# Kernel tuning notes

Measured on AMD Instinct MI355X. Metric: run time of the kernel, lower is better.

The kernel has to match this reference:

```python
import jax, jax.numpy as jnp
import numpy as np

STEP, LEAK = 16, 32
KS = STEP + LEAK          # kernel_size = 48
FODEP = KS                # forced depression window
SYNAPSES, NEURONS = 64, 256
IC, OC = 1, 10
DENSE = 0.5
THETA = DENSE * SYNAPSES * IC   # 32.0
BIAS = 0.5
BATCH, TIME = 16, 512


def setup_inputs() -> dict:
    key = jax.random.key(0)
    k1, k2 = jax.random.split(key)
    # binary input spikes, density 0.2
    input_spikes = (jax.random.uniform(k1, (BATCH, IC, SYNAPSES, TIME)) < 0.2).astype(jnp.float32)
    # weight ~ Exponential(rate=1/w_init=2).sample().clip(0,1), mean 0.5
    u = jax.random.uniform(k2, (OC * NEURONS, IC * SYNAPSES), minval=1e-6, maxval=1.0)
    weight = jnp.clip(-0.5 * jnp.log(u), 0.0, 1.0)
    return {"input_spikes": input_spikes, "weight": weight}


def _step_fire_leak_kernel(weight):
    # kernel[o, i, t] = max(0, min(t/step, -(t - w*step)/leak + w)), flipped on t
    t = jnp.arange(KS, dtype=weight.dtype)
    t_spike = t / STEP                                        # rising edge
    t_leak = -(t - weight[..., None] * STEP) / LEAK + weight[..., None]  # decaying edge
    kernel = jnp.maximum(jnp.zeros((), weight.dtype), jnp.minimum(t_spike, t_leak))
    return kernel[..., ::-1]


def _forward(input_spikes, weight):
    B, C, S, T = input_spikes.shape
    x = input_spikes.reshape(B, C * S, T)
    kernel = _step_fire_leak_kernel(weight)                   # [OC*N, IC*S, KS]
    # conv1d with padding = kernel_size on both sides -> T' = T + KS + 1
    pot = jax.lax.conv_general_dilated(
        x, kernel, window_strides=(1,), padding=[(KS, KS)],
        dimension_numbers=("NCH", "OIH", "NCH"))
    Tp = pot.shape[-1]
    pot = pot.reshape(B, OC, NEURONS, Tp) + BIAS * THETA      # unsupervised bias path

    # winner-takes-all scan over time with per-(batch, neuron) depression counter
    pot_t = pot.transpose(3, 0, 2, 1)                         # [T', B, N, OC]
    dep0 = jnp.zeros((B, NEURONS, OC), jnp.int32)

    def step_fn(dep, p):
        masked = jnp.where(dep == 0, p, jnp.zeros((), p.dtype))
        winner = jnp.argmax(masked, axis=-1)                  # [B, N]
        wpot = jnp.take_along_axis(masked, winner[..., None], axis=-1)[..., 0]
        spike = (wpot > THETA).astype(p.dtype)                # [B, N]
        w_t = jax.nn.one_hot(winner, OC, dtype=p.dtype) * spike[..., None]
        dep = jnp.clip(dep + spike.astype(jnp.int32)[..., None] * FODEP - 1, 0, FODEP - 1)
        return dep, w_t

    _, winners = jax.lax.scan(step_fn, dep0, pot_t)           # [T', B, N, OC]
    return winners.transpose(1, 3, 2, 0)                      # [B, OC, N, T'] float


def reference(input_spikes, weight):
    return _forward(input_spikes, weight)
```

## Files before the change

### kernel.cpp

```cpp
#include <hip/hip_runtime.h>

#define B_   16
#define OC_  10
#define N_   256
#define O_   2560
#define S_   64
#define T_   512
#define KS_  48
#define TP_  561
#define TT   24
#define WROW 72

#define XROWS 624
#define SCH    16
#define CPITCH 572
#define KP     18

using i32x4 = __attribute__((ext_vector_type(4))) int;

__global__ void prep_all(const float* __restrict__ x, const float* __restrict__ w,
                         unsigned char* __restrict__ xb, signed char* __restrict__ Bg) {
    if (blockIdx.x < 512) {
#pragma unroll
        for (int it = 0; it < 4; ++it) {
            int idx = blockIdx.x * 256 + threadIdx.x + it * 131072;
            int t = idx & 511;
            int bi = idx >> 9;
            int i = bi & 63, b = bi >> 6;
            xb[((size_t)(b * 512 + t) << 6) + i] = (x[idx] != 0.0f) ? 1 : 0;
        }
    } else {
        int base = (blockIdx.x - 512) * 256 + threadIdx.x;
#pragma unroll
        for (int it = 0; it < 16; ++it) {
            int idx = base + it * 491520;
            int i = idx & 63;
            int oj = idx >> 6;
            int j = oj % KS_, o = oj / KS_;
            float wv = w[(o << 6) + i];
            float rise = (float)j * 0.0625f;
            float leak = -((float)j - wv * 16.0f) * 0.03125f + wv;
            float kv   = fmaxf(0.0f, fminf(rise, leak));
            int q  = (int)lrintf(kv * 4194304.0f);
            int d0 = ((q + 128) & 255) - 128;
            int q1 = (q - d0) >> 8;
            int d1 = ((q1 + 128) & 255) - 128;
            int d2 = (q1 - d1) >> 8;
            int oc = o >> 4, ol = o & 15;
            int jm = j & 15, jh = j >> 4;
            int pos = jm * 3 + jh;
            size_t bse = (((size_t)(oc * KS_ + pos) * 48) + ol) * 64 + i;
            Bg[bse]            = (signed char)d0;
            Bg[bse + 16 * 64]  = (signed char)d1;
            Bg[bse + 32 * 64]  = (signed char)d2;
        }
    }
}

__global__ __launch_bounds__(512, 2) void gemm_scan(
    const unsigned char* __restrict__ xb,
    const signed char*  __restrict__ Bg,
    float* __restrict__ out)
{
    __shared__ __align__(16) unsigned char smem[143616];
    unsigned char* xT    = smem;
    unsigned char* codeW = smem;
    float*         keyBB = (float*)(smem + 39936);
    unsigned char* codeBB = smem + 39936 + 82944;

    const int tid  = threadIdx.x;
    const int lane = tid & 63;
    const int wave = tid >> 6;
    const int tq   = wave >> 1;
    const int chh  = wave & 1;
    const int nc = blockIdx.x;
    const int b  = blockIdx.y;
    const int lrow = lane & 15;
    const int quad = lane >> 4;
    const int tw = tq * 144;

    float*         keyB  = keyBB + chh * (576 * KP);
    unsigned char* codeB = codeBB + chh * (576 * KP);

    const size_t SL = (size_t)KS_ * 48 * 64;
    const signed char* Bcur = Bg + (size_t)(chh * 80 + nc) * SL
                            + lrow * 64 + quad * 16;

    for (int z = tid; z < 112 * 4; z += 512) {
        int zi = z >> 2, p = z & 3;
        int r = (zi < 49) ? zi : (561 + zi - 49);
        *(i32x4*)(xT + r * 64 + p * 16) = (i32x4){0, 0, 0, 0};
    }
    const unsigned char* xbb = xb + ((size_t)b << 15);
    for (int q = tid; q < 2048; q += 512) {
        i32x4 v = *(const i32x4*)(xbb + q * 16);
        int t = q >> 2, p = q & 3;
        int r = 49 + t;
        *(i32x4*)(xT + r * 64 + ((p ^ ((r >> 1) & 3)) << 4)) = v;
    }

    i32x4 acc[9][3];
    i32x4 af[11], bfA[9], bfB[9];

#pragma unroll
    for (int jh = 0; jh < 3; ++jh)
#pragma unroll
        for (int f = 0; f < 3; ++f)
            bfA[jh * 3 + f] = *(const i32x4*)(Bcur + jh * 3072 + f * 1024);

    __syncthreads();

    {
        const int rb0 = tw + 16 + lrow;
        const int ca0 = ((quad ^ ((rb0 >> 1) & 3)) << 4);
#pragma unroll
        for (int k = 0; k < 11; ++k)
            af[k] = *(const i32x4*)(xT + (rb0 + k * 16) * 64 + ca0);
    }

#define MF(bfC, mi, jh, f)                                                    \
    acc[mi][f] = __builtin_amdgcn_mfma_i32_16x16x64_i8(                       \
        af[(mi) + 2 - (jh)], bfC[(jh) * 3 + (f)], acc[mi][f], 0, 0, 0)

#define PAIR(bfC, m0)                                                         \
    MF(bfC, m0, 0, 0); MF(bfC, m0, 0, 1); MF(bfC, m0, 0, 2);                  \
    MF(bfC, (m0)+1, 0, 0); MF(bfC, (m0)+1, 0, 1); MF(bfC, (m0)+1, 0, 2);      \
    MF(bfC, m0, 1, 0); MF(bfC, m0, 1, 1); MF(bfC, m0, 1, 2);                  \
    MF(bfC, (m0)+1, 1, 0); MF(bfC, (m0)+1, 1, 1); MF(bfC, (m0)+1, 1, 2);      \
    MF(bfC, m0, 2, 0); MF(bfC, m0, 2, 1); MF(bfC, m0, 2, 2);                  \
    MF(bfC, (m0)+1, 2, 0); MF(bfC, (m0)+1, 2, 1); MF(bfC, (m0)+1, 2, 2);

#define PAIR9(bfC)                                                            \
    MF(bfC, 8, 0, 0); MF(bfC, 8, 0, 1); MF(bfC, 8, 0, 2);                     \
    MF(bfC, 8, 1, 0); MF(bfC, 8, 1, 1); MF(bfC, 8, 1, 2);                     \
    MF(bfC, 8, 2, 0); MF(bfC, 8, 2, 1); MF(bfC, 8, 2, 2);

#define LDA_(row) (*(const i32x4*)(xT + (row) * 64 + coffN))
#define LDB_(BP, jh, f) (*(const i32x4*)((BP) + (tn3 + (jh)) * 3072 + (f) * 1024))

#define TLOC(T, bfC, bfN, BP) {                                               \
        const int rbn   = tw + 16 - (((T) + 1) & 15) + lrow;                  \
        const int coffN = ((quad ^ ((rbn >> 1) & 3)) << 4);                   \
        const int tn3   = (((T) + 1) & 15) * 3;                               \
        __builtin_amdgcn_s_setprio(1);                                        \
        PAIR(bfC, 0)                                                          \
        af[0] = LDA_(rbn);        af[1] = LDA_(rbn + 16);                     \
        bfN[0] = LDB_(BP, 0, 0); bfN[1] = LDB_(BP, 0, 1); bfN[2] = LDB_(BP, 0, 2); \
        PAIR(bfC, 2)                                                          \
        af[2] = LDA_(rbn + 32);   af[3] = LDA_(rbn + 48);                     \
        bfN[3] = LDB_(BP, 1, 0); bfN[4] = LDB_(BP, 1, 1); bfN[5] = LDB_(BP, 1, 2); \
        PAIR(bfC, 4)                                                          \
        af[4] = LDA_(rbn + 64);   af[5] = LDA_(rbn + 80);                     \
        bfN[6] = LDB_(BP, 2, 0); bfN[7] = LDB_(BP, 2, 1); bfN[8] = LDB_(BP, 2, 2); \
        PAIR(bfC, 6)                                                          \
        af[6] = LDA_(rbn + 96);   af[7] = LDA_(rbn + 112);                    \
        PAIR9(bfC)                                                            \
        af[8] = LDA_(rbn + 128);  af[9] = LDA_(rbn + 144);                    \
        af[10] = LDA_(rbn + 160);                                             \
        __builtin_amdgcn_s_setprio(0);                                        \
    }

    for (int c = 0; c < 5; ++c) {
        const signed char* Bnxt = (c == 4) ? Bcur : (Bcur + 16 * SL);

#pragma unroll
        for (int mi = 0; mi < 9; ++mi)
#pragma unroll
            for (int f = 0; f < 3; ++f)
                acc[mi][f] = (i32x4){0, 0, 0, 0};

        for (int tp = 0; tp < 7; ++tp) {
            TLOC(2 * tp,     bfA, bfB, Bcur)
            TLOC(2 * tp + 1, bfB, bfA, Bcur)
        }
        TLOC(14, bfA, bfB, Bcur)
        TLOC(15, bfB, bfA, Bnxt)

        {
            const unsigned char cv = (unsigned char)(chh * 5 + c + 1);
#pragma unroll
            for (int mi = 0; mi < 9; ++mi) {
#pragma unroll
                for (int r = 0; r < 4; ++r) {
                    int t = tw + mi * 16 + quad * 4 + r;
                    int pq_i = acc[mi][0][r] + (acc[mi][1][r] << 8)
                             + (acc[mi][2][r] << 16);
                    float pq = (float)pq_i * 2.384185791015625e-7f;
                    int ix = t * KP + lrow;
                    if (c == 0) {
                        keyB[ix] = pq; codeB[ix] = cv;
                    } else if (pq > keyB[ix]) {
                        keyB[ix] = pq; codeB[ix] = cv;
                    }
                }
            }
        }
        Bcur = Bnxt;
    }

#undef MF
#undef PAIR
#undef PAIR9
#undef LDA_
#undef LDB_
#undef TLOC

    __syncthreads();

    for (int ix = tid; ix < 576 * 16; ix += 512) {
        int t = ix >> 4, nl = ix & 15;
        if (t >= TP_) continue;
        int ip = t * KP + nl;
        float f0 = keyBB[ip];
        float f1 = keyBB[576 * KP + ip];
        float best = f0;
        unsigned char cd = codeBB[ip];
        if (f1 > f0) { best = f1; cd = codeBB[576 * KP + ip]; }
        codeW[nl * CPITCH + t] = ((best + 16.0f) > 32.0f) ? cd : (unsigned char)0;
    }
    __syncthreads();

    {
        const int ln = tid & 63;
        float* ob = out + (((size_t)b * OC_) * N_ + nc * SCH) * TP_;
        for (int nsel = wave; nsel < SCH; nsel += 8) {
            const unsigned char* cp = &codeW[nsel * CPITCH];
            int t = 0;
            while (t < TP_) {
                int tt = t + ln;
                unsigned char v = (tt < TP_) ? cp[tt] : (unsigned char)0;
                unsigned long long mask = __ballot(v != 0);
                if (mask == 0ULL) { t += 64; continue; }
                int k = (int)__builtin_ctzll(mask);
                if (ln == k)
                    ob[((size_t)(v - 1) * N_ + nsel) * TP_ + (t + k)] = 1.0f;
                t += k + KS_;
            }
        }
    }
}

__global__ void transpose_w(const float* __restrict__ w, float* __restrict__ wT) {
    int idx = blockIdx.x * 256 + threadIdx.x;
    if (idx >= O_ * S_) return;
    int o = idx >> 6, i = idx & 63;
    wT[i * O_ + o] = w[idx];
}

__global__ __launch_bounds__(256) void conv_kernel(
    const float* __restrict__ x, const float* __restrict__ wT,
    float* __restrict__ pot)
{
    const int b  = blockIdx.y;
    const int t0 = blockIdx.z * TT;
    const int o  = blockIdx.x * 256 + threadIdx.x;

    __shared__ __align__(16) float xsh[S_][WROW];
    for (int idx = threadIdx.x; idx < S_ * WROW; idx += 256) {
        int i = idx / WROW, m = idx - i * WROW;
        int t = t0 - KS_ + m;
        float v = 0.0f;
        if (t >= 0 && t < T_) v = x[(b * S_ + i) * T_ + t];
        xsh[i][m] = v;
    }
    __syncthreads();

    float acch[TT], accl[TT];
#pragma unroll
    for (int tl = 0; tl < TT; ++tl) { acch[tl] = 0.0f; accl[tl] = 0.0f; }

    for (int i = 0; i < S_; ++i) {
        float xw[WROW];
#pragma unroll
        for (int w4 = 0; w4 < WROW / 4; ++w4) {
            const float4 v = *reinterpret_cast<const float4*>(&xsh[i][w4 * 4]);
            xw[w4 * 4 + 0] = v.x; xw[w4 * 4 + 1] = v.y;
            xw[w4 * 4 + 2] = v.z; xw[w4 * 4 + 3] = v.w;
        }
        const float wv = wT[i * O_ + o];
#pragma unroll
        for (int j = 1; j < KS_; ++j) {
            float rise = (float)j * 0.0625f;
            float leak = -((float)j - wv * 16.0f) * 0.03125f + wv;
            float kv   = fmaxf(0.0f, fminf(rise, leak));
            float khi  = rintf(kv * 4096.0f) * 2.44140625e-4f;
            float klo  = kv - khi;
#pragma unroll
            for (int tl = 0; tl < TT; ++tl) {
                float xv = xw[tl + (KS_ - 1) - j];
                acch[tl] = fmaf(xv, khi, acch[tl]);
                accl[tl] = fmaf(xv, klo, accl[tl]);
            }
        }
    }
#pragma unroll
    for (int tl = 0; tl < TT; ++tl) {
        int t = t0 + tl;
        if (t < TP_) pot[((size_t)b * TP_ + t) * O_ + o] = acch[tl] + accl[tl];
    }
}

__global__ void scan_prep(const float* __restrict__ pot, unsigned char* __restrict__ code) {
    int idx = blockIdx.x * 256 + threadIdx.x;
    if (idx >= B_ * TP_ * N_) return;
    int n  = idx & (N_ - 1);
    int bt = idx >> 8;
    const float* p = pot + (size_t)bt * O_ + n;
    float best = p[0]; int bo = 0;
#pragma unroll
    for (int oc = 1; oc < OC_; ++oc) {
        float v = p[oc * N_];
        if (v > best) { best = v; bo = oc; }
    }
    code[idx] = ((best + 16.0f) > 32.0f) ? (unsigned char)(bo + 1) : (unsigned char)0;
}

__global__ void scan_run(const unsigned char* __restrict__ code, float* __restrict__ out) {
    int idx = blockIdx.x * 256 + threadIdx.x;
    if (idx >= B_ * N_) return;
    int b = idx >> 8, n = idx & 255;
    const unsigned char* c = code + (size_t)b * TP_ * N_ + n;
    int t = 0;
    while (t < TP_) {
        unsigned char buf[KS_];
#pragma unroll
        for (int k = 0; k < KS_; ++k) {
            int tt = t + k;
            buf[k] = (tt < TP_) ? c[(size_t)tt * N_] : (unsigned char)0;
        }
        int adv = KS_;
#pragma unroll
        for (int k = 0; k < KS_; ++k) {
            if (buf[k]) {
                out[(((size_t)b * OC_ + (buf[k] - 1)) * N_ + n) * TP_ + (t + k)] = 1.0f;
                adv = k + KS_;
                break;
            }
        }
        t += adv;
    }
}

extern "C" void kernel_launch(void* const* d_in, const int* in_sizes, int n_in,
                              void* d_out, int out_size, void* d_ws, size_t ws_size,
                              hipStream_t stream) {
    const float* x = (const float*)d_in[0];
    const float* w = (const float*)d_in[1];
    float* out = (float*)d_out;

    char* ws = (char*)d_ws;
    const size_t szX = (size_t)B_ * T_ * S_;
    const size_t szB = (size_t)160 * KS_ * 48 * 64;
    const size_t need = szX + szB;

    if (ws_size >= need) {
        unsigned char* xb  = (unsigned char*)ws;
        signed char* Bg    = (signed char*)(ws + szX);

        hipMemsetAsync(d_out, 0, (size_t)out_size * sizeof(float), stream);
        prep_all<<<2432, 256, 0, stream>>>(x, w, xb, Bg);
        gemm_scan<<<dim3(16, 16), 512, 0, stream>>>(xb, Bg, out);
    } else {
        size_t pot_bytes  = (size_t)B_ * TP_ * O_ * sizeof(float);
        size_t code_bytes = (size_t)B_ * TP_ * N_;
        float* pot = (float*)ws;
        unsigned char* code = (unsigned char*)(ws + pot_bytes);
        float* wT = (float*)(ws + pot_bytes + code_bytes);

        hipMemsetAsync(d_out, 0, (size_t)out_size * sizeof(float), stream);
        transpose_w<<<(O_ * S_ + 255) / 256, 256, 0, stream>>>(w, wT);
        conv_kernel<<<dim3(O_ / 256, B_, (TP_ + TT - 1) / TT), 256, 0, stream>>>(x, wT, pot);
        scan_prep<<<(B_ * TP_ * N_ + 255) / 256, 256, 0, stream>>>(pot, code);
        scan_run<<<(B_ * N_ + 255) / 256, 256, 0, stream>>>(code, out);
    }
}
```

Before: 238.9 us.

## Overlap per-chunk epilogue with next chunk MFMAs and fold output zeroing into prep

The max/argmax epilogue over accumulators for chunk c is moved into the first time-tile of chunk c+1, interleaved with MFMA pairs so LDS compare/store work overlaps with matrix math. keyB is now pre-initialized to a large negative value so every chunk uses the same compare path, and the final chunk's epilogue runs after the loop. Separately, the hipMemsetAsync of the output is replaced by extra blocks in prep_all that zero the output with vector stores, removing one launch. The interleaving raises register pressure and depends on the scheduler actually overlapping the work.

```diff
diff --git a/kernel.cpp b/kernel.cpp
--- a/kernel.cpp
+++ b/kernel.cpp
@@ -16,10 +16,13 @@
 #define CPITCH 572
 #define KP     18
 
+#define OUTF4  5744640
+
 using i32x4 = __attribute__((ext_vector_type(4))) int;
 
 __global__ void prep_all(const float* __restrict__ x, const float* __restrict__ w,
-                         unsigned char* __restrict__ xb, signed char* __restrict__ Bg) {
+                         unsigned char* __restrict__ xb, signed char* __restrict__ Bg,
+                         float* __restrict__ outz) {
     if (blockIdx.x < 512) {
 #pragma unroll
         for (int it = 0; it < 4; ++it) {
@@ -29,7 +32,7 @@
             int i = bi & 63, b = bi >> 6;
             xb[((size_t)(b * 512 + t) << 6) + i] = (x[idx] != 0.0f) ? 1 : 0;
         }
-    } else {
+    } else if (blockIdx.x < 2432) {
         int base = (blockIdx.x - 512) * 256 + threadIdx.x;
 #pragma unroll
         for (int it = 0; it < 16; ++it) {
@@ -54,6 +57,14 @@
             Bg[bse + 16 * 64]  = (signed char)d1;
             Bg[bse + 32 * 64]  = (signed char)d2;
         }
+    } else {
+        i32x4* o4 = (i32x4*)outz;
+        int base = (blockIdx.x - 2432) * 256 + threadIdx.x;
+#pragma unroll
+        for (int it = 0; it < 8; ++it) {
+            int idx = base + it * 737280;
+            if (idx < OUTF4) o4[idx] = (i32x4){0, 0, 0, 0};
+        }
     }
 }
 
@@ -86,6 +97,12 @@
     const signed char* Bcur = Bg + (size_t)(chh * 80 + nc) * SL
                             + lrow * 64 + quad * 16;
 
+#pragma unroll
+    for (int mi = 0; mi < 9; ++mi)
+#pragma unroll
+        for (int r = 0; r < 4; ++r)
+            keyB[(tw + mi * 16 + quad * 4 + r) * KP + lrow] = -1.0e30f;
+
     for (int z = tid; z < 112 * 4; z += 512) {
         int zi = z >> 2, p = z & 3;
         int r = (zi < 49) ? zi : (561 + zi - 49);
@@ -137,6 +154,20 @@
 
 #define LDA_(row) (*(const i32x4*)(xT + (row) * 64 + coffN))
 #define LDB_(BP, jh, f) (*(const i32x4*)((BP) + (tn3 + (jh)) * 3072 + (f) * 1024))
+
+#define EPR(mi, r) {                                                          \
+        int t_ = tw + (mi) * 16 + quad * 4 + (r);                             \
+        int pq_i = acc[mi][0][r] + (acc[mi][1][r] << 8)                       \
+                 + (acc[mi][2][r] << 16);                                     \
+        float pq = (float)pq_i * 2.384185791015625e-7f;                       \
+        int ix_ = t_ * KP + lrow;                                             \
+        if (pq > keyB[ix_]) { keyB[ix_] = pq; codeB[ix_] = cvp; }             \
+    }
+#define EP(mi) EPR(mi, 0) EPR(mi, 1) EPR(mi, 2) EPR(mi, 3)
+
+#define ZAC(mi) acc[mi][0] = (i32x4){0,0,0,0};                                \
+                acc[mi][1] = (i32x4){0,0,0,0};                                \
+                acc[mi][2] = (i32x4){0,0,0,0};
 
 #define TLOC(T, bfC, bfN, BP) {                                               \
         const int rbn   = tw + 16 - (((T) + 1) & 15) + lrow;                  \
@@ -160,42 +191,66 @@
         __builtin_amdgcn_s_setprio(0);                                        \
     }
 
+#define TLOC0_EP() {                                                          \
+        const int rbn   = tw + 16 - 1 + lrow;                                 \
+        const int coffN = ((quad ^ ((rbn >> 1) & 3)) << 4);                   \
+        const int tn3   = 3;                                                  \
+        const unsigned char cvp = (unsigned char)(chh * 5 + c);               \
+        EP(0) EP(1) ZAC(0) ZAC(1)                                             \
+        __builtin_amdgcn_s_setprio(1); PAIR(bfA, 0)                           \
+        __builtin_amdgcn_s_setprio(0);                                        \
+        af[0] = LDA_(rbn);        af[1] = LDA_(rbn + 16);                     \
+        bfB[0] = LDB_(Bcur, 0, 0); bfB[1] = LDB_(Bcur, 0, 1);                 \
+        bfB[2] = LDB_(Bcur, 0, 2);                                            \
+        EP(2) EP(3) ZAC(2) ZAC(3)                                             \
+        __builtin_amdgcn_s_setprio(1); PAIR(bfA, 2)                           \
+        __builtin_amdgcn_s_setprio(0);                                        \
+        af[2] = LDA_(rbn + 32);   af[3] = LDA_(rbn + 48);                     \
+        bfB[3] = LDB_(Bcur, 1, 0); bfB[4] = LDB_(Bcur, 1, 1);                 \
+        bfB[5] = LDB_(Bcur, 1, 2);                                            \
+        EP(4) EP(5) ZAC(4) ZAC(5)                                             \
+        __builtin_amdgcn_s_setprio(1); PAIR(bfA, 4)                           \
+        __builtin_amdgcn_s_setprio(0);                                        \
+        af[4] = LDA_(rbn + 64);   af[5] = LDA_(rbn + 80);                     \
+        bfB[6] = LDB_(Bcur, 2, 0); bfB[7] = LDB_(Bcur, 2, 1);                 \
+        bfB[8] = LDB_(Bcur, 2, 2);                                            \
+        EP(6) EP(7) ZAC(6) ZAC(7)                                             \
+        __builtin_amdgcn_s_setprio(1); PAIR(bfA, 6)                           \
+        __builtin_amdgcn_s_setprio(0);                                        \
+        af[6] = LDA_(rbn + 96);   af[7] = LDA_(rbn + 112);                    \
+        EP(8) ZAC(8)                                                          \
+        __builtin_amdgcn_s_setprio(1); PAIR9(bfA)                             \
+        __builtin_amdgcn_s_setprio(0);                                        \
+        af[8] = LDA_(rbn + 128);  af[9] = LDA_(rbn + 144);                    \
+        af[10] = LDA_(rbn + 160);                                             \
+    }
+
     for (int c = 0; c < 5; ++c) {
         const signed char* Bnxt = (c == 4) ? Bcur : (Bcur + 16 * SL);
 
-#pragma unroll
-        for (int mi = 0; mi < 9; ++mi)
-#pragma unroll
-            for (int f = 0; f < 3; ++f)
-                acc[mi][f] = (i32x4){0, 0, 0, 0};
-
-        for (int tp = 0; tp < 7; ++tp) {
+        if (c == 0) {
+#pragma unroll
+            for (int mi = 0; mi < 9; ++mi)
+#pragma unroll
+                for (int f = 0; f < 3; ++f)
+                    acc[mi][f] = (i32x4){0, 0, 0, 0};
+            TLOC(0, bfA, bfB, Bcur)
+        } else {
+            TLOC0_EP()
+        }
+        TLOC(1, bfB, bfA, Bcur)
+        for (int tp = 1; tp < 7; ++tp) {
             TLOC(2 * tp,     bfA, bfB, Bcur)
             TLOC(2 * tp + 1, bfB, bfA, Bcur)
         }
         TLOC(14, bfA, bfB, Bcur)
         TLOC(15, bfB, bfA, Bnxt)
-
-        {
-            const unsigned char cv = (unsigned char)(chh * 5 + c + 1);
-#pragma unroll
-            for (int mi = 0; mi < 9; ++mi) {
-#pragma unroll
-                for (int r = 0; r < 4; ++r) {
-                    int t = tw + mi * 16 + quad * 4 + r;
-                    int pq_i = acc[mi][0][r] + (acc[mi][1][r] << 8)
-                             + (acc[mi][2][r] << 16);
-                    float pq = (float)pq_i * 2.384185791015625e-7f;
-                    int ix = t * KP + lrow;
-                    if (c == 0) {
-                        keyB[ix] = pq; codeB[ix] = cv;
-                    } else if (pq > keyB[ix]) {
-                        keyB[ix] = pq; codeB[ix] = cv;
-                    }
-                }
-            }
-        }
         Bcur = Bnxt;
+    }
+
+    {
+        const unsigned char cvp = (unsigned char)(chh * 5 + 5);
+        EP(0) EP(1) EP(2) EP(3) EP(4) EP(5) EP(6) EP(7) EP(8)
     }
 
 #undef MF
@@ -203,7 +258,11 @@
 #undef PAIR9
 #undef LDA_
 #undef LDB_
+#undef EPR
+#undef EP
+#undef ZAC
 #undef TLOC
+#undef TLOC0_EP
 
     __syncthreads();
 
@@ -357,8 +416,7 @@
         unsigned char* xb  = (unsigned char*)ws;
         signed char* Bg    = (signed char*)(ws + szX);
 
-        hipMemsetAsync(d_out, 0, (size_t)out_size * sizeof(float), stream);
-        prep_all<<<2432, 256, 0, stream>>>(x, w, xb, Bg);
+        prep_all<<<5312, 256, 0, stream>>>(x, w, xb, Bg, out);
         gemm_scan<<<dim3(16, 16), 512, 0, stream>>>(xb, Bg, out);
     } else {
         size_t pot_bytes  = (size_t)B_ * TP_ * O_ * sizeof(float);
```

Result: slower. 267.2 us (+11.9%).
